# Kernel tuning notes

Hardware: AMD Instinct MI355X
Metric: run time of the kernel (lower is better)

Reference implementation:

```python
import jax, jax.numpy as jnp
import numpy as np

# dims (must match input_specs / init_kwargs)
T, B_SZ, K, OBS_LAST = 512, 8, 128, 2
OBS_DIM = K * OBS_LAST          # 256
N_ACTIONS = 64
N_UNITS, N_FEAT = 256, 8
D_INNER = N_UNITS * N_FEAT      # 2048
H, N_STATE = 16, 64             # p_heads, state_size
P = D_INNER // H                # headdim = 128


def setup_inputs() -> dict:
    key = jax.random.key(0)
    ks = jax.random.split(key, 12)
    s = lambda fan_in: 1.0 / np.sqrt(fan_in)
    return {
        "obs": jax.random.normal(ks[0], (T, B_SZ, K, OBS_LAST), jnp.float32),
        # input projection obs_dim -> d_inner
        "W_in": jax.random.normal(ks[1], (OBS_DIM, D_INNER), jnp.float32) * s(OBS_DIM),
        "b_in": jnp.zeros((D_INNER,), jnp.float32),
        # SSD cell params (Mamba2-style)
        "A_log": jnp.log(jnp.linspace(1.0, 16.0, H).astype(jnp.float32)),
        "dt_bias": jnp.full((H,), -2.0, jnp.float32),
        "W_dt": jax.random.normal(ks[2], (D_INNER, H), jnp.float32) * s(D_INNER),
        "W_B": jax.random.normal(ks[3], (D_INNER, H * N_STATE), jnp.float32) * s(D_INNER),
        "W_C": jax.random.normal(ks[4], (D_INNER, H * N_STATE), jnp.float32) * s(D_INNER),
        # SSD output projection d_inner -> n_units
        "W_yo": jax.random.normal(ks[5], (D_INNER, N_UNITS), jnp.float32) * s(D_INNER),
        "b_yo": jnp.zeros((N_UNITS,), jnp.float32),
        # policy head n_units -> n_actions
        "W_head": jax.random.normal(ks[6], (N_UNITS, N_ACTIONS), jnp.float32) * s(N_UNITS),
        "b_head": jnp.zeros((N_ACTIONS,), jnp.float32),
    }


def _ssd_scan(x, A_log, dt_bias, W_dt, W_B, W_C):
    # x: (T, B, D_INNER) -> y: (T, B, D_INNER) via selective state-space scan
    t, b, _ = x.shape
    dt = jax.nn.softplus(jnp.einsum("tbd,dh->tbh", x, W_dt) + dt_bias)   # (T,B,H)
    Bm = jnp.einsum("tbd,dm->tbm", x, W_B).reshape(t, b, H, N_STATE)      # (T,B,H,N)
    Cm = jnp.einsum("tbd,dm->tbm", x, W_C).reshape(t, b, H, N_STATE)      # (T,B,H,N)
    xh = x.reshape(t, b, H, P)                                            # (T,B,H,P)
    decay = jnp.exp(-jnp.exp(A_log)[None, None, :] * dt)                  # (T,B,H)

    def step(h, inp):
        dec_t, dt_t, B_t, C_t, x_t = inp
        # h: (B,H,P,N); rank-1 input update per head
        h = dec_t[:, :, None, None] * h + dt_t[:, :, None, None] * jnp.einsum(
            "bhp,bhn->bhpn", x_t, B_t)
        y = jnp.einsum("bhpn,bhn->bhp", h, C_t)                           # (B,H,P)
        return h, y

    h0 = jnp.zeros((b, H, P, N_STATE), x.dtype)
    _, ys = jax.lax.scan(step, h0, (decay, dt, Bm, Cm, xh))
    return ys.reshape(t, b, D_INNER)


def reference(obs, W_in, b_in, A_log, dt_bias, W_dt, W_B, W_C, W_yo, b_yo, W_head, b_head):
    t, b = obs.shape[0], obs.shape[1]
    flat = obs.reshape(t * b, -1)                                 # (t*B, obs_dim)
    x = jax.nn.relu(flat @ W_in + b_in).reshape(t, b, D_INNER)     # (t,B,d_inner)
    y = _ssd_scan(x, A_log, dt_bias, W_dt, W_B, W_C)               # (t,B,d_inner)
    hid = jnp.einsum("tbd,du->tbu", y, W_yo) + b_yo                # (t,B,n_units)
    z = jax.nn.relu(hid).reshape(t * b, N_UNITS)
    logits = z @ W_head + b_head
    return logits.reshape(t, b, N_ACTIONS)
```

## Files before the change

### kernel.cpp

```cpp
#include <hip/hip_runtime.h>
#include <cstdint>
#include <cstddef>

typedef unsigned short u16;
typedef __attribute__((ext_vector_type(8))) __bf16 bf16x8;
typedef __attribute__((ext_vector_type(4))) float floatx4;

#define T_DIM   512
#define B_SZ    8
#define ROWS    4096
#define OBS_D   256
#define D_IN    2048
#define NHEAD   16
#define NSTATE  64
#define PDIM    128
#define NUNITS  256
#define NACT    64
#define NSEG    4
#define SEGT    128
#define SLOT    (B_SZ * NHEAD * PDIM * NSTATE)

__host__ __device__ __forceinline__ float bf2f(u16 u) {
    union { uint32_t i; float f; } v; v.i = ((uint32_t)u) << 16; return v.f;
}
__host__ __device__ __forceinline__ u16 f2bf(float f) {
    union { float f; uint32_t i; } v; v.f = f;
    uint32_t r = v.i + 0x7FFFu + ((v.i >> 16) & 1u);
    return (u16)(r >> 16);
}

__device__ __forceinline__ void glds16(const u16* g, u16* l) {
    __builtin_amdgcn_global_load_lds(
        (__attribute__((address_space(1))) void*)g,
        (__attribute__((address_space(3))) void*)l, 16, 0, 0);
}

__global__ __launch_bounds__(256) void ActorAgent_27625229647898_kernel(
        float* __restrict__ out, int n, float v) {
    for (int i = blockIdx.x * 256 + threadIdx.x; i < n; i += gridDim.x * 256)
        out[i] = v;
}

__global__ __launch_bounds__(256) void prep(const float* __restrict__ obs,
                                            const float* __restrict__ W_dt,
                                            const float* __restrict__ W_in,
                                            const float* __restrict__ W_B,
                                            const float* __restrict__ W_C,
                                            const float* __restrict__ W_yo,
                                            const float* __restrict__ W_head,
                                            u16* __restrict__ obsb, u16* __restrict__ Wdtb,
                                            u16* __restrict__ WinT, u16* __restrict__ WBCT,
                                            u16* __restrict__ WyoT, u16* __restrict__ WheadT) {
    int bid = blockIdx.x;
    if (bid < 160) {
        const int NOBS = ROWS * OBS_D;
        const int NDT  = D_IN * NHEAD;
        for (int i = bid * 256 + threadIdx.x; i < NOBS + NDT; i += 160 * 256) {
            if (i < NOBS) obsb[i] = f2bf(obs[i]);
            else          Wdtb[i - NOBS] = f2bf(W_dt[i - NOBS]);
        }
        return;
    }
    bid -= 160;
    const float* src; u16* dst; int R, C, bx, by;
    if (bid < 512)       { src = W_in;   dst = WinT;   R = 256;  C = 2048; bx = bid & 63; by = bid >> 6; }
    else if (bid < 2560) { int i = bid - 512;  src = W_B;  dst = WBCT; R = 2048; C = 1024; bx = i & 31; by = i >> 5; }
    else if (bid < 4608) { int i = bid - 2560; src = W_C;  dst = WBCT + (size_t)1024 * 2048; R = 2048; C = 1024; bx = i & 31; by = i >> 5; }
    else if (bid < 5120) { int i = bid - 4608; src = W_yo; dst = WyoT; R = 2048; C = 256;  bx = i & 7;  by = i >> 3; }
    else                 { int i = bid - 5120; src = W_head; dst = WheadT; R = 256; C = 64; bx = i & 1; by = i >> 1; }
    __shared__ float t[32][33];
    int c0 = bx * 32, r0 = by * 32;
    int tx = threadIdx.x & 31, ty = threadIdx.x >> 5;
#pragma unroll
    for (int i = 0; i < 32; i += 8)
        t[ty + i][tx] = src[(size_t)(r0 + ty + i) * C + c0 + tx];
    __syncthreads();
#pragma unroll
    for (int i = 0; i < 32; i += 8)
        dst[(size_t)(c0 + ty + i) * R + r0 + tx] = f2bf(t[tx][ty + i]);
}

template <int ACT, int OUT_BF16, int HAS_BIAS>
__global__ __launch_bounds__(256) void gemm_bt128(const u16* __restrict__ A,
                                                  const u16* __restrict__ BT,
                                                  const float* __restrict__ bias,
                                                  void* __restrict__ Cout,
                                                  int M, int N, int K) {
    __shared__ __align__(16) u16 sA[128 * 64];
    __shared__ __align__(16) u16 sB[128 * 64];
    const int tid  = threadIdx.x;
    const int wave = tid >> 6, lane = tid & 63;
    const int quad = lane >> 4, lr = lane & 15;
    const int wm = wave & 1, wn = wave >> 1;
    const int m0 = blockIdx.x * 128, n0 = blockIdx.y * 128;
    const int srl = lane >> 3, sc = (lane & 7) * 8;

    floatx4 acc[4][4];
#pragma unroll
    for (int i = 0; i < 4; i++)
#pragma unroll
        for (int j = 0; j < 4; j++)
#pragma unroll
            for (int r = 0; r < 4; r++) acc[i][j][r] = 0.f;

    const u16* apg = A + (size_t)(m0 + wave * 32 + srl) * K + sc;
    const u16* bpg = BT + (size_t)(n0 + wave * 32 + srl) * K + sc;

    for (int k0 = 0; k0 < K; k0 += 64) {
        __syncthreads();
#pragma unroll
        for (int g = 0; g < 4; ++g) {
            glds16(apg + (size_t)(g * 8) * K + k0, &sA[(wave * 32 + g * 8) * 64]);
            glds16(bpg + (size_t)(g * 8) * K + k0, &sB[(wave * 32 + g * 8) * 64]);
        }
        __syncthreads();
#pragma unroll
        for (int ks = 0; ks < 2; ++ks) {
            bf16x8 af[4], bfr[4];
#pragma unroll
            for (int i = 0; i < 4; i++)
                af[i] = *(const bf16x8*)&sA[(wm * 64 + i * 16 + lr) * 64 + ks * 32 + quad * 8];
#pragma unroll
            for (int j = 0; j < 4; j++)
                bfr[j] = *(const bf16x8*)&sB[(wn * 64 + j * 16 + lr) * 64 + ks * 32 + quad * 8];
#pragma unroll
            for (int i = 0; i < 4; i++)
#pragma unroll
                for (int j = 0; j < 4; j++)
                    acc[i][j] = __builtin_amdgcn_mfma_f32_16x16x32_bf16(af[i], bfr[j], acc[i][j], 0, 0, 0);
        }
    }
#pragma unroll
    for (int j = 0; j < 4; j++) {
        int col = n0 + wn * 64 + j * 16 + lr;
        float bvv = HAS_BIAS ? bias[col] : 0.f;
#pragma unroll
        for (int i = 0; i < 4; i++) {
#pragma unroll
            for (int r = 0; r < 4; r++) {
                int row = m0 + wm * 64 + i * 16 + quad * 4 + r;
                float v = acc[i][j][r] + bvv;
                if (ACT) v = fmaxf(v, 0.f);
                if (OUT_BF16) ((u16*)Cout)[(size_t)row * N + col] = f2bf(v);
                else          ((float*)Cout)[(size_t)row * N + col] = v;
            }
        }
    }
}

template <int ACT, int OUT_BF16>
__global__ __launch_bounds__(256) void gemm_bt64(const u16* __restrict__ A,
                                                 const u16* __restrict__ BT,
                                                 const float* __restrict__ bias,
                                                 void* __restrict__ Cout,
                                                 int M, int N, int K) {
    __shared__ __align__(16) u16 sA[64 * 64];
    __shared__ __align__(16) u16 sB[64 * 64];
    const int tid  = threadIdx.x;
    const int wave = tid >> 6, lane = tid & 63;
    const int quad = lane >> 4, lr = lane & 15;
    const int m0 = blockIdx.x * 64, n0 = blockIdx.y * 64;
    const int srl = lane >> 3, sc = (lane & 7) * 8;

    floatx4 acc[4];
#pragma unroll
    for (int i = 0; i < 4; i++)
#pragma unroll
        for (int j = 0; j < 4; j++) acc[i][j] = 0.f;

    const u16* apg = A + (size_t)(m0 + wave * 16 + srl) * K + sc;
    const u16* bpg = BT + (size_t)(n0 + wave * 16 + srl) * K + sc;

    for (int k0 = 0; k0 < K; k0 += 64) {
        __syncthreads();
#pragma unroll
        for (int g = 0; g < 2; ++g) {
            glds16(apg + (size_t)(g * 8) * K + k0, &sA[(wave * 16 + g * 8) * 64]);
            glds16(bpg + (size_t)(g * 8) * K + k0, &sB[(wave * 16 + g * 8) * 64]);
        }
        __syncthreads();
#pragma unroll
        for (int ks = 0; ks < 2; ++ks) {
            bf16x8 af = *(const bf16x8*)&sA[(wave * 16 + lr) * 64 + ks * 32 + quad * 8];
#pragma unroll
            for (int nt = 0; nt < 4; nt++) {
                bf16x8 bf = *(const bf16x8*)&sB[(nt * 16 + lr) * 64 + ks * 32 + quad * 8];
                acc[nt] = __builtin_amdgcn_mfma_f32_16x16x32_bf16(af, bf, acc[nt], 0, 0, 0);
            }
        }
    }
#pragma unroll
    for (int nt = 0; nt < 4; nt++) {
        int col = n0 + nt * 16 + lr;
        float bvv = bias ? bias[col] : 0.f;
#pragma unroll
        for (int r = 0; r < 4; r++) {
            int row = m0 + wave * 16 + quad * 4 + r;
            float v = acc[nt][r] + bvv;
            if (ACT) v = fmaxf(v, 0.f);
            if (OUT_BF16) ((u16*)Cout)[(size_t)row * N + col] = f2bf(v);
            else          ((float*)Cout)[(size_t)row * N + col] = v;
        }
    }
}

__global__ __launch_bounds__(256) void dt_kernel(const u16* __restrict__ xb,
                                                 const u16* __restrict__ Wdtb,
                                                 const float* __restrict__ dt_bias,
                                                 const float* __restrict__ A_log,
                                                 float* __restrict__ dtv,
                                                 float* __restrict__ decayv) {
    const int row = blockIdx.x;
    __shared__ __align__(16) u16 xr[D_IN];
    __shared__ float part[256];
    const int tid = threadIdx.x;
    *(uint4*)&xr[tid * 8] = *(const uint4*)(xb + (size_t)row * D_IN + tid * 8);
    __syncthreads();
    const int h = tid & 15, ks = tid >> 4;
    float acc = 0.f;
    const int kb = ks * 128;
    for (int k = 0; k < 128; ++k)
        acc = fmaf(bf2f(xr[kb + k]), bf2f(Wdtb[(size_t)(kb + k) * NHEAD + h]), acc);
    part[tid] = acc;
    __syncthreads();
    if (tid < 16) {
        float s = 0.f;
        for (int k2 = 0; k2 < 16; ++k2) s += part[k2 * 16 + tid];
        float z = s + dt_bias[tid];
        float sp = (z > 20.f) ? z : log1pf(expf(z));
        float a = expf(A_log[tid]);
        dtv[row * NHEAD + tid]    = sp;
        decayv[row * NHEAD + tid] = expf(-a * sp);
    }
}

__global__ __launch_bounds__(256) void seg_state(const u16* __restrict__ xw,
                                                 const u16* __restrict__ BCm,
                                                 const float* __restrict__ dtv,
                                                 const float* __restrict__ decayv,
                                                 float* __restrict__ Hbuf) {
    const int blk = blockIdx.x;
    const int seg = blk >> 7;
    const int b   = (blk >> 4) & 7;
    const int h   = blk & 15;
    const int tid = threadIdx.x;
    const int pgrp = tid >> 3;
    const int oct  = tid & 7;

    __shared__ __align__(16) u16 sx[SEGT][PDIM];
    __shared__ __align__(16) u16 sbm[SEGT][NSTATE];
    __shared__ float sw[SEGT];
    __shared__ float sdt[SEGT];
    __shared__ float sdec[SEGT];
    __shared__ float sP[32];

    const int t0 = seg * SEGT;

#pragma unroll
    for (int k = 0; k < 8; ++k) {
        int idx = tid + k * 256;
        int t = idx >> 4, c = (idx & 15) * 8;
        int r = (t0 + t) * B_SZ + b;
        *(uint4*)&sx[t][c] = *(const uint4*)(xw + (size_t)r * D_IN + h * PDIM + c);
    }
#pragma unroll
    for (int k = 0; k < 4; ++k) {
        int idx = tid + k * 256;
        int t = idx >> 3, c = (idx & 7) * 8;
        int r = (t0 + t) * B_SZ + b;
        *(uint4*)&sbm[t][c] = *(const uint4*)(BCm + (size_t)r * D_IN + h * NSTATE + c);
    }
    if (tid < SEGT)            sdt[tid] = dtv[((t0 + tid) * B_SZ + b) * NHEAD + h];
    else if (tid < 2 * SEGT)   sdec[tid - SEGT] = decayv[((t0 + tid - SEGT) * B_SZ + b) * NHEAD + h];
    __syncthreads();

    if (tid < 32) {
        float p = 1.f;
        for (int i = 3; i >= 0; --i) {
            int t = tid * 4 + i;
            sw[t] = sdt[t] * p;
            p *= sdec[t];
        }
        sP[tid] = p;
    }
    __syncthreads();
    if (tid == 0) {
        float suf = 1.f;
        for (int q = 31; q >= 0; --q) { float tmp = sP[q]; sP[q] = suf; suf *= tmp; }
    }
    __syncthreads();
    if (tid < 32) {
        float m = sP[tid];
        for (int i = 0; i < 4; ++i) sw[tid * 4 + i] *= m;
    }
    __syncthreads();

    float acc[4][8];
#pragma unroll
    for (int i = 0; i < 4; i++)
#pragma unroll
        for (int j = 0; j < 8; j++) acc[i][j] = 0.f;

    for (int t = 0; t < SEGT; ++t) {
        float w = sw[t];
        const u16* xp = &sx[t][pgrp * 4];
        const u16* bp = &sbm[t][oct * 8];
        float xv[4], bv[8];
#pragma unroll
        for (int i = 0; i < 4; i++) xv[i] = w * bf2f(xp[i]);
#pragma unroll
        for (int j = 0; j < 8; j++) bv[j] = bf2f(bp[j]);
#pragma unroll
        for (int i = 0; i < 4; i++)
#pragma unroll
            for (int j = 0; j < 8; j++)
                acc[i][j] = fmaf(xv[i], bv[j], acc[i][j]);
    }

    float* base = Hbuf + (size_t)seg * SLOT +
                  (((size_t)b * NHEAD + h) * PDIM + pgrp * 4) * NSTATE + oct * 8;
#pragma unroll
    for (int i = 0; i < 4; i++) {
        *(float4*)(base + (size_t)i * NSTATE)     = make_float4(acc[i][0], acc[i][1], acc[i][2], acc[i][3]);
        *(float4*)(base + (size_t)i * NSTATE + 4) = make_float4(acc[i][4], acc[i][5], acc[i][6], acc[i][7]);
    }
}

__global__ __launch_bounds__(256) void seg_prefix(const float* __restrict__ Hbuf,
                                                  const float* __restrict__ decayv,
                                                  u16* __restrict__ Hbf) {
    const int blk = blockIdx.x;
    const int b  = blk >> 6;
    const int h  = (blk >> 2) & 15;
    const int ec = blk & 3;
    const int tid = threadIdx.x;

    __shared__ float sA[NSEG];

    if (tid < 64 * (NSEG - 2)) {
        int s = 1 + (tid >> 6);
        int i = tid & 63;
        int t = s * SEGT + i * 2;
        float p = decayv[(t * B_SZ + b) * NHEAD + h] *
                  decayv[((t + 1) * B_SZ + b) * NHEAD + h];
        p *= __shfl_xor(p, 1);
        p *= __shfl_xor(p, 2);
        p *= __shfl_xor(p, 4);
        p *= __shfl_xor(p, 8);
        p *= __shfl_xor(p, 16);
        p *= __shfl_xor(p, 32);
        if (i == 0) sA[s] = p;
    }
    __syncthreads();

    const size_t base = (((size_t)b * NHEAD + h) * PDIM * NSTATE) + (size_t)ec * 2048 + tid * 8;
    float4 P0 = *(const float4*)(Hbuf + base);
    float4 P1 = *(const float4*)(Hbuf + base + 4);
    u16 pk[8];
    pk[0] = f2bf(P0.x); pk[1] = f2bf(P0.y); pk[2] = f2bf(P0.z); pk[3] = f2bf(P0.w);
    pk[4] = f2bf(P1.x); pk[5] = f2bf(P1.y); pk[6] = f2bf(P1.z); pk[7] = f2bf(P1.w);
    *(uint4*)(Hbf + base) = *(const uint4*)pk;
#pragma unroll
    for (int s = 1; s <= NSEG - 2; ++s) {
        float a = sA[s];
        const float* slot = Hbuf + (size_t)s * SLOT + base;
        float4 h0 = *(const float4*)(slot);
        float4 h1 = *(const float4*)(slot + 4);
        P0.x = fmaf(a, P0.x, h0.x); P0.y = fmaf(a, P0.y, h0.y);
        P0.z = fmaf(a, P0.z, h0.z); P0.w = fmaf(a, P0.w, h0.w);
        P1.x = fmaf(a, P1.x, h1.x); P1.y = fmaf(a, P1.y, h1.y);
        P1.z = fmaf(a, P1.z, h1.z); P1.w = fmaf(a, P1.w, h1.w);
        pk[0] = f2bf(P0.x); pk[1] = f2bf(P0.y); pk[2] = f2bf(P0.z); pk[3] = f2bf(P0.w);
        pk[4] = f2bf(P1.x); pk[5] = f2bf(P1.y); pk[6] = f2bf(P1.z); pk[7] = f2bf(P1.w);
        *(uint4*)(Hbf + (size_t)s * SLOT + base) = *(const uint4*)pk;
    }
}

__global__ __launch_bounds__(256) void chunk_scan(const u16* __restrict__ BCm,
                                                  const float* __restrict__ dtv,
                                                  const float* __restrict__ decayv,
                                                  const u16* __restrict__ Hbf,
                                                  u16* __restrict__ xb) {
    __shared__ __align__(16) u16 sB_[128][68];
    __shared__ __align__(16) u16 sC_[128][68];
    __shared__ __align__(16) u16 sS[128][132];
    __shared__ __align__(16) u16 sXT[128][36];
    __shared__ float sdt[SEGT], sL[SEGT], sEL[SEGT], stmp[32];

    const int blk = blockIdx.x;
    const int seg = blk >> 7, b = (blk >> 4) & 7, h = blk & 15;
    const int tid = threadIdx.x;
    const int wave = tid >> 6, lane = tid & 63;
    const int quad = lane >> 4, lr = lane & 15;
    const int wm = wave & 1, wn = wave >> 1;
    const int t0 = seg * SEGT;

#pragma unroll
    for (int it = 0; it < 4; ++it) {
        int idx = tid + it * 256;
        int t = idx >> 3, c = (idx & 7) * 8;
        int r = (t0 + t) * B_SZ + b;
        *(uint4*)&sB_[t][c] = *(const uint4*)(BCm + (size_t)r * D_IN + h * NSTATE + c);
        *(uint4*)&sC_[t][c] = *(const uint4*)(BCm + (size_t)r * D_IN + 1024 + h * NSTATE + c);
    }
    if (tid < SEGT) sdt[tid] = dtv[((t0 + tid) * B_SZ + b) * NHEAD + h];
    else if (tid < 2 * SEGT) {
        int t = tid - SEGT;
        sL[t] = __logf(fmaxf(decayv[((t0 + t) * B_SZ + b) * NHEAD + h], 1e-30f));
    }
    __syncthreads();
    if (tid < 32) {
        float s = 0.f, v[4];
#pragma unroll
        for (int i = 0; i < 4; ++i) { s += sL[tid * 4 + i]; v[i] = s; }
        stmp[tid] = s;
#pragma unroll
        for (int i = 0; i < 4; ++i) sL[tid * 4 + i] = v[i];
    }
    __syncthreads();
    if (tid == 0) {
        float run = 0.f;
        for (int q = 0; q < 32; ++q) { float c2 = stmp[q]; stmp[q] = run; run += c2; }
    }
    __syncthreads();
    if (tid < 32) {
        float off = stmp[tid];
#pragma unroll
        for (int i = 0; i < 4; ++i) sL[tid * 4 + i] += off;
    }
    __syncthreads();
    if (tid < SEGT) sEL[tid] = __expf(sL[tid]);

    floatx4 accS[4][4];
#pragma unroll
    for (int i = 0; i < 4; i++)
#pragma unroll
        for (int j = 0; j < 4; j++)
#pragma unroll
            for (int r = 0; r < 4; r++) accS[i][j][r] = 0.f;
#pragma unroll
    for (int k0 = 0; k0 < 64; k0 += 32) {
        bf16x8 af[4], bfr[4];
#pragma unroll
        for (int i = 0; i < 4; i++)
            af[i] = *(const bf16x8*)&sB_[wm * 64 + i * 16 + lr][k0 + quad * 8];
#pragma unroll
        for (int j = 0; j < 4; j++)
            bfr[j] = *(const bf16x8*)&sC_[wn * 64 + j * 16 + lr][k0 + quad * 8];
#pragma unroll
        for (int i = 0; i < 4; i++)
#pragma unroll
            for (int j = 0; j < 4; j++)
                accS[i][j] = __builtin_amdgcn_mfma_f32_16x16x32_bf16(af[i], bfr[j], accS[i][j], 0, 0, 0);
    }
#pragma unroll
    for (int j = 0; j < 4; j++) {
        int tt = wn * 64 + j * 16 + lr;
        float Lt = sL[tt];
#pragma unroll
        for (int i = 0; i < 4; i++) {
#pragma unroll
            for (int r = 0; r < 4; r++) {
                int tp = wm * 64 + i * 16 + quad * 4 + r;
                float v = 0.f;
                if (tp <= tt) v = accS[i][j][r] * sdt[tp] * __expf(Lt - sL[tp]);
                sS[tt][tp] = f2bf(v);
            }
        }
    }

    floatx4 acc[4][4];
#pragma unroll
    for (int i = 0; i < 4; i++)
#pragma unroll
        for (int j = 0; j < 4; j++)
#pragma unroll
            for (int r = 0; r < 4; r++) acc[i][j][r] = 0.f;
    __syncthreads();
    if (seg > 0) {
        const u16* hbase = Hbf + (size_t)(seg - 1) * SLOT + (((size_t)b * NHEAD + h) * PDIM) * NSTATE;
#pragma unroll
        for (int k0 = 0; k0 < 64; k0 += 32) {
            bf16x8 af[4], bfr[4];
#pragma unroll
            for (int i = 0; i < 4; i++)
                af[i] = *(const bf16x8*)&sC_[wm * 64 + i * 16 + lr][k0 + quad * 8];
#pragma unroll
            for (int j = 0; j < 4; j++)
                bfr[j] = *(const bf16x8*)(hbase + (size_t)(wn * 64 + j * 16 + lr) * NSTATE + k0 + quad * 8);
#pragma unroll
            for (int i = 0; i < 4; i++)
#pragma unroll
                for (int j = 0; j < 4; j++)
                    acc[i][j] = __builtin_amdgcn_mfma_f32_16x16x32_bf16(af[i], bfr[j], acc[i][j], 0, 0, 0);
        }
#pragma unroll
        for (int i = 0; i < 4; i++) {
#pragma unroll
            for (int r = 0; r < 4; r++) {
                float el = sEL[wm * 64 + i * 16 + quad * 4 + r];
#pragma unroll
                for (int j = 0; j < 4; j++) acc[i][j][r] *= el;
            }
        }
    }

    const int px = tid & 127, koh = (tid >> 7) * 16;
    for (int kc = 0; kc < 128; kc += 32) {
        u16 xv[16];
#pragma unroll
        for (int j2 = 0; j2 < 16; ++j2) {
            int tp = kc + koh + j2;
            xv[j2] = xb[(size_t)((t0 + tp) * B_SZ + b) * D_IN + h * PDIM + px];
        }
        __syncthreads();
        *(uint4*)&sXT[px][koh]     = *(const uint4*)&xv[0];
        *(uint4*)&sXT[px][koh + 8] = *(const uint4*)&xv[8];
        __syncthreads();
        bf16x8 af[4], bfr[4];
#pragma unroll
        for (int i = 0; i < 4; i++)
            af[i] = *(const bf16x8*)&sS[wm * 64 + i * 16 + lr][kc + quad * 8];
#pragma unroll
        for (int j = 0; j < 4; j++)
            bfr[j] = *(const bf16x8*)&sXT[wn * 64 + j * 16 + lr][quad * 8];
#pragma unroll
        for (int i = 0; i < 4; i++)
#pragma unroll
            for (int j = 0; j < 4; j++)
                acc[i][j] = __builtin_amdgcn_mfma_f32_16x16x32_bf16(af[i], bfr[j], acc[i][j], 0, 0, 0);
    }

#pragma unroll
    for (int j = 0; j < 4; j++) {
        int p = wn * 64 + j * 16 + lr;
#pragma unroll
        for (int i = 0; i < 4; i++) {
#pragma unroll
            for (int r = 0; r < 4; r++) {
                int t = wm * 64 + i * 16 + quad * 4 + r;
                xb[(size_t)((t0 + t) * B_SZ + b) * D_IN + h * PDIM + p] = f2bf(acc[i][j][r]);
            }
        }
    }
}

extern "C" void kernel_launch(void* const* d_in, const int* in_sizes, int n_in,
                              void* d_out, int out_size, void* d_ws, size_t ws_size,
                              hipStream_t stream) {
    const float* obs     = (const float*)d_in[0];
    const float* W_in    = (const float*)d_in[1];
    const float* b_in    = (const float*)d_in[2];
    const float* A_log   = (const float*)d_in[3];
    const float* dt_bias = (const float*)d_in[4];
    const float* W_dt    = (const float*)d_in[5];
    const float* W_B     = (const float*)d_in[6];
    const float* W_C     = (const float*)d_in[7];
    const float* W_yo    = (const float*)d_in[8];
    const float* b_yo    = (const float*)d_in[9];
    const float* W_head  = (const float*)d_in[10];
    const float* b_head  = (const float*)d_in[11];

    char* ws = (char*)d_ws;
    size_t o = 0;
    u16*   xb     = (u16*)(ws + o);   o += (size_t)ROWS * D_IN * 2;
    u16*   BCm    = (u16*)(ws + o);   o += (size_t)ROWS * D_IN * 2;
    float* dtv    = (float*)(ws + o); o += (size_t)ROWS * NHEAD * 4;
    float* decayv = (float*)(ws + o); o += (size_t)ROWS * NHEAD * 4;
    u16*   zb     = (u16*)(ws + o);   o += (size_t)ROWS * NUNITS * 2;
    float* Hseg   = (float*)(ws + o); o += (size_t)(NSEG - 1) * SLOT * 4;
    u16*   Hbf    = (u16*)(ws + o);   o += (size_t)(NSEG - 1) * SLOT * 2;
    u16*   obsb   = (u16*)(ws + o);   o += (size_t)ROWS * OBS_D * 2;
    u16*   WinT   = (u16*)(ws + o);   o += (size_t)D_IN * OBS_D * 2;
    u16*   WBCT   = (u16*)(ws + o);   o += (size_t)D_IN * D_IN * 2;
    u16*   WyoT   = (u16*)(ws + o);   o += (size_t)NUNITS * D_IN * 2;
    u16*   WheadT = (u16*)(ws + o);   o += (size_t)NACT * NUNITS * 2;
    u16*   Wdtb   = (u16*)(ws + o);   o += (size_t)D_IN * NHEAD * 2;

    ActorAgent_27625229647898_kernel<<<dim3(1), 256, 0, stream>>>((float*)d_out, 0, 0.f);

    prep<<<dim3(160 + 5136), 256, 0, stream>>>(obs, W_dt, W_in, W_B, W_C, W_yo, W_head,
                                               obsb, Wdtb, WinT, WBCT, WyoT, WheadT);

    gemm_bt128<1, 1, 1><<<dim3(32, 16), 256, 0, stream>>>(obsb, WinT, b_in, xb, ROWS, D_IN, OBS_D);
    dt_kernel<<<dim3(ROWS), 256, 0, stream>>>(xb, Wdtb, dt_bias, A_log, dtv, decayv);
    gemm_bt128<0, 1, 0><<<dim3(32, 16), 256, 0, stream>>>(xb, WBCT, (const float*)nullptr, BCm, ROWS, D_IN, D_IN);
    seg_state<<<dim3((NSEG - 1) * 128), 256, 0, stream>>>(xb, BCm, dtv, decayv, Hseg);
    seg_prefix<<<dim3(512), 256, 0, stream>>>(Hseg, decayv, Hbf);
    chunk_scan<<<dim3(NSEG * 128), 256, 0, stream>>>(BCm, dtv, decayv, Hbf, xb);
    gemm_bt64<1, 1><<<dim3(64, 4), 256, 0, stream>>>(xb, WyoT, b_yo, zb, ROWS, NUNITS, D_IN);
    gemm_bt64<0, 0><<<dim3(64, 1), 256, 0, stream>>>(zb, WheadT, b_head, (float*)d_out, ROWS, NACT, NUNITS);
}
```

Baseline: 254.4 us.

## Fuse dt projection into B/C GEMM and shrink GEMM tile to 128x64

Appends the W_dt columns (zero-padded to a stride of 2112) to the concatenated B/C weight matrix, so the big GEMM also produces the dt pre-activations. This replaces the per-row dt_kernel with a small elementwise dt_fix kernel that applies softplus and decay. The GEMM kernel tile also changes from 128x128 with K-step 64 to 128x64 with K-step 32, doubling the block count for more parallelism but adding more barriers per unit of work. The dt values now come from a bf16-rounded GEMM output, which slightly changes precision, and the padded row stride adds some wasted compute.

```diff
diff --git a/kernel.cpp b/kernel.cpp
--- a/kernel.cpp
+++ b/kernel.cpp
@@ -19,6 +19,7 @@
 #define NSEG    4
 #define SEGT    128
 #define SLOT    (B_SZ * NHEAD * PDIM * NSTATE)
+#define BCSTR   2112
 
 __host__ __device__ __forceinline__ float bf2f(u16 u) {
     union { uint32_t i; float f; } v; v.i = ((uint32_t)u) << 16; return v.f;
@@ -48,16 +49,23 @@
                                             const float* __restrict__ W_C,
                                             const float* __restrict__ W_yo,
                                             const float* __restrict__ W_head,
-                                            u16* __restrict__ obsb, u16* __restrict__ Wdtb,
+                                            u16* __restrict__ obsb,
                                             u16* __restrict__ WinT, u16* __restrict__ WBCT,
                                             u16* __restrict__ WyoT, u16* __restrict__ WheadT) {
     int bid = blockIdx.x;
     if (bid < 160) {
         const int NOBS = ROWS * OBS_D;
         const int NDT  = D_IN * NHEAD;
-        for (int i = bid * 256 + threadIdx.x; i < NOBS + NDT; i += 160 * 256) {
+        const int NZ   = 48 * D_IN;
+        for (int i = bid * 256 + threadIdx.x; i < NOBS + NDT + NZ; i += 160 * 256) {
             if (i < NOBS) obsb[i] = f2bf(obs[i]);
-            else          Wdtb[i - NOBS] = f2bf(W_dt[i - NOBS]);
+            else if (i < NOBS + NDT) {
+                int j = i - NOBS;
+                int k = j >> 4, n = j & 15;
+                WBCT[(size_t)(2048 + n) * D_IN + k] = f2bf(W_dt[j]);
+            } else {
+                WBCT[(size_t)2064 * D_IN + (i - NOBS - NDT)] = 0;
+            }
         }
         return;
     }
@@ -81,58 +89,56 @@
 }
 
 template <int ACT, int OUT_BF16, int HAS_BIAS>
-__global__ __launch_bounds__(256) void gemm_bt128(const u16* __restrict__ A,
-                                                  const u16* __restrict__ BT,
-                                                  const float* __restrict__ bias,
-                                                  void* __restrict__ Cout,
-                                                  int M, int N, int K) {
-    __shared__ __align__(16) u16 sA[128 * 64];
-    __shared__ __align__(16) u16 sB[128 * 64];
+__global__ __launch_bounds__(256) void gemm_bt(const u16* __restrict__ A,
+                                               const u16* __restrict__ BT,
+                                               const float* __restrict__ bias,
+                                               void* __restrict__ Cout,
+                                               int M, int N, int K) {
+    __shared__ __align__(16) u16 sA[128 * 32];
+    __shared__ __align__(16) u16 sB[64 * 32];
     const int tid  = threadIdx.x;
     const int wave = tid >> 6, lane = tid & 63;
     const int quad = lane >> 4, lr = lane & 15;
     const int wm = wave & 1, wn = wave >> 1;
-    const int m0 = blockIdx.x * 128, n0 = blockIdx.y * 128;
-    const int srl = lane >> 3, sc = (lane & 7) * 8;
-
-    floatx4 acc[4][4];
+    const int m0 = blockIdx.x * 128, n0 = blockIdx.y * 64;
+    const int srl = lane >> 2, sc = (lane & 3) * 8;
+
+    floatx4 acc[4][2];
 #pragma unroll
     for (int i = 0; i < 4; i++)
 #pragma unroll
-        for (int j = 0; j < 4; j++)
+        for (int j = 0; j < 2; j++)
 #pragma unroll
             for (int r = 0; r < 4; r++) acc[i][j][r] = 0.f;
 
     const u16* apg = A + (size_t)(m0 + wave * 32 + srl) * K + sc;
-    const u16* bpg = BT + (size_t)(n0 + wave * 32 + srl) * K + sc;
-
-    for (int k0 = 0; k0 < K; k0 += 64) {
+    const u16* bpg = BT + (size_t)(n0 + wave * 16 + srl) * K + sc;
+    u16* lA0 = &sA[(wave * 32) * 32];
+    u16* lA1 = &sA[(wave * 32 + 16) * 32];
+    u16* lB  = &sB[(wave * 16) * 32];
+
+    for (int k0 = 0; k0 < K; k0 += 32) {
         __syncthreads();
-#pragma unroll
-        for (int g = 0; g < 4; ++g) {
-            glds16(apg + (size_t)(g * 8) * K + k0, &sA[(wave * 32 + g * 8) * 64]);
-            glds16(bpg + (size_t)(g * 8) * K + k0, &sB[(wave * 32 + g * 8) * 64]);
-        }
+        glds16(apg + k0, lA0);
+        glds16(apg + (size_t)16 * K + k0, lA1);
+        glds16(bpg + k0, lB);
         __syncthreads();
-#pragma unroll
-        for (int ks = 0; ks < 2; ++ks) {
-            bf16x8 af[4], bfr[4];
-#pragma unroll
-            for (int i = 0; i < 4; i++)
-                af[i] = *(const bf16x8*)&sA[(wm * 64 + i * 16 + lr) * 64 + ks * 32 + quad * 8];
-#pragma unroll
-            for (int j = 0; j < 4; j++)
-                bfr[j] = *(const bf16x8*)&sB[(wn * 64 + j * 16 + lr) * 64 + ks * 32 + quad * 8];
-#pragma unroll
-            for (int i = 0; i < 4; i++)
-#pragma unroll
-                for (int j = 0; j < 4; j++)
-                    acc[i][j] = __builtin_amdgcn_mfma_f32_16x16x32_bf16(af[i], bfr[j], acc[i][j], 0, 0, 0);
-        }
-    }
-#pragma unroll
-    for (int j = 0; j < 4; j++) {
-        int col = n0 + wn * 64 + j * 16 + lr;
+        bf16x8 af[4], bfr[2];
+#pragma unroll
+        for (int i = 0; i < 4; i++)
+            af[i] = *(const bf16x8*)&sA[(wm * 64 + i * 16 + lr) * 32 + quad * 8];
+#pragma unroll
+        for (int j = 0; j < 2; j++)
+            bfr[j] = *(const bf16x8*)&sB[(wn * 32 + j * 16 + lr) * 32 + quad * 8];
+#pragma unroll
+        for (int i = 0; i < 4; i++)
+#pragma unroll
+            for (int j = 0; j < 2; j++)
+                acc[i][j] = __builtin_amdgcn_mfma_f32_16x16x32_bf16(af[i], bfr[j], acc[i][j], 0, 0, 0);
+    }
+#pragma unroll
+    for (int j = 0; j < 2; j++) {
+        int col = n0 + wn * 32 + j * 16 + lr;
         float bvv = HAS_BIAS ? bias[col] : 0.f;
 #pragma unroll
         for (int i = 0; i < 4; i++) {
@@ -204,34 +210,17 @@
     }
 }
 
-__global__ __launch_bounds__(256) void dt_kernel(const u16* __restrict__ xb,
-                                                 const u16* __restrict__ Wdtb,
-                                                 const float* __restrict__ dt_bias,
-                                                 const float* __restrict__ A_log,
-                                                 float* __restrict__ dtv,
-                                                 float* __restrict__ decayv) {
-    const int row = blockIdx.x;
-    __shared__ __align__(16) u16 xr[D_IN];
-    __shared__ float part[256];
-    const int tid = threadIdx.x;
-    *(uint4*)&xr[tid * 8] = *(const uint4*)(xb + (size_t)row * D_IN + tid * 8);
-    __syncthreads();
-    const int h = tid & 15, ks = tid >> 4;
-    float acc = 0.f;
-    const int kb = ks * 128;
-    for (int k = 0; k < 128; ++k)
-        acc = fmaf(bf2f(xr[kb + k]), bf2f(Wdtb[(size_t)(kb + k) * NHEAD + h]), acc);
-    part[tid] = acc;
-    __syncthreads();
-    if (tid < 16) {
-        float s = 0.f;
-        for (int k2 = 0; k2 < 16; ++k2) s += part[k2 * 16 + tid];
-        float z = s + dt_bias[tid];
-        float sp = (z > 20.f) ? z : log1pf(expf(z));
-        float a = expf(A_log[tid]);
-        dtv[row * NHEAD + tid]    = sp;
-        decayv[row * NHEAD + tid] = expf(-a * sp);
-    }
+__global__ __launch_bounds__(256) void dt_fix(const u16* __restrict__ BCm,
+                                              const float* __restrict__ dt_bias,
+                                              const float* __restrict__ A_log,
+                                              float* __restrict__ dtv,
+                                              float* __restrict__ decayv) {
+    int i = blockIdx.x * 256 + threadIdx.x;
+    int row = i >> 4, h = i & 15;
+    float z = bf2f(BCm[(size_t)row * BCSTR + 2048 + h]) + dt_bias[h];
+    float sp = (z > 20.f) ? z : log1pf(expf(z));
+    dtv[i] = sp;
+    decayv[i] = expf(-expf(A_log[h]) * sp);
 }
 
 __global__ __launch_bounds__(256) void seg_state(const u16* __restrict__ xw,
@@ -268,7 +257,7 @@
         int idx = tid + k * 256;
         int t = idx >> 3, c = (idx & 7) * 8;
         int r = (t0 + t) * B_SZ + b;
-        *(uint4*)&sbm[t][c] = *(const uint4*)(BCm + (size_t)r * D_IN + h * NSTATE + c);
+        *(uint4*)&sbm[t][c] = *(const uint4*)(BCm + (size_t)r * BCSTR + h * NSTATE + c);
     }
     if (tid < SEGT)            sdt[tid] = dtv[((t0 + tid) * B_SZ + b) * NHEAD + h];
     else if (tid < 2 * SEGT)   sdec[tid - SEGT] = decayv[((t0 + tid - SEGT) * B_SZ + b) * NHEAD + h];
@@ -400,8 +389,8 @@
         int idx = tid + it * 256;
         int t = idx >> 3, c = (idx & 7) * 8;
         int r = (t0 + t) * B_SZ + b;
-        *(uint4*)&sB_[t][c] = *(const uint4*)(BCm + (size_t)r * D_IN + h * NSTATE + c);
-        *(uint4*)&sC_[t][c] = *(const uint4*)(BCm + (size_t)r * D_IN + 1024 + h * NSTATE + c);
+        *(uint4*)&sB_[t][c] = *(const uint4*)(BCm + (size_t)r * BCSTR + h * NSTATE + c);
+        *(uint4*)&sC_[t][c] = *(const uint4*)(BCm + (size_t)r * BCSTR + 1024 + h * NSTATE + c);
     }
     if (tid < SEGT) sdt[tid] = dtv[((t0 + tid) * B_SZ + b) * NHEAD + h];
     else if (tid < 2 * SEGT) {
@@ -564,7 +553,7 @@
     char* ws = (char*)d_ws;
     size_t o = 0;
     u16*   xb     = (u16*)(ws + o);   o += (size_t)ROWS * D_IN * 2;
-    u16*   BCm    = (u16*)(ws + o);   o += (size_t)ROWS * D_IN * 2;
+    u16*   BCm    = (u16*)(ws + o);   o += (size_t)ROWS * BCSTR * 2;
     float* dtv    = (float*)(ws + o); o += (size_t)ROWS * NHEAD * 4;
     float* decayv = (float*)(ws + o); o += (size_t)ROWS * NHEAD * 4;
     u16*   zb     = (u16*)(ws + o);   o += (size_t)ROWS * NUNITS * 2;
@@ -572,19 +561,18 @@
     u16*   Hbf    = (u16*)(ws + o);   o += (size_t)(NSEG - 1) * SLOT * 2;
     u16*   obsb   = (u16*)(ws + o);   o += (size_t)ROWS * OBS_D * 2;
     u16*   WinT   = (u16*)(ws + o);   o += (size_t)D_IN * OBS_D * 2;
-    u16*   WBCT   = (u16*)(ws + o);   o += (size_t)D_IN * D_IN * 2;
+    u16*   WBCT   = (u16*)(ws + o);   o += (size_t)BCSTR * D_IN * 2;
     u16*   WyoT   = (u16*)(ws + o);   o += (size_t)NUNITS * D_IN * 2;
     u16*   WheadT = (u16*)(ws + o);   o += (size_t)NACT * NUNITS * 2;
-    u16*   Wdtb   = (u16*)(ws + o);   o += (size_t)D_IN * NHEAD * 2;
 
     ActorAgent_27625229647898_kernel<<<dim3(1), 256, 0, stream>>>((float*)d_out, 0, 0.f);
 
     prep<<<dim3(160 + 5136), 256, 0, stream>>>(obs, W_dt, W_in, W_B, W_C, W_yo, W_head,
-                                               obsb, Wdtb, WinT, WBCT, WyoT, WheadT);
-
-    gemm_bt128<1, 1, 1><<<dim3(32, 16), 256, 0, stream>>>(obsb, WinT, b_in, xb, ROWS, D_IN, OBS_D);
-    dt_kernel<<<dim3(ROWS), 256, 0, stream>>>(xb, Wdtb, dt_bias, A_log, dtv, decayv);
-    gemm_bt128<0, 1, 0><<<dim3(32, 16), 256, 0, stream>>>(xb, WBCT, (const float*)nullptr, BCm, ROWS, D_IN, D_IN);
+                                               obsb, WinT, WBCT, WyoT, WheadT);
+
+    gemm_bt<1, 1, 1><<<dim3(32, 32), 256, 0, stream>>>(obsb, WinT, b_in, xb, ROWS, D_IN, OBS_D);
+    gemm_bt<0, 1, 0><<<dim3(32, 33), 256, 0, stream>>>(xb, WBCT, (const float*)nullptr, BCm, ROWS, BCSTR, D_IN);
+    dt_fix<<<dim3(256), 256, 0, stream>>>(BCm, dt_bias, A_log, dtv, decayv);
     seg_state<<<dim3((NSEG - 1) * 128), 256, 0, stream>>>(xb, BCm, dtv, decayv, Hseg);
     seg_prefix<<<dim3(512), 256, 0, stream>>>(Hseg, decayv, Hbf);
     chunk_scan<<<dim3(NSEG * 128), 256, 0, stream>>>(BCm, dtv, decayv, Hbf, xb);
```

New measurement: 251.3 us. No clear change (-1.2%).
